# Kernel optimization log

Hardware: AMD Instinct MI355X
Metric: run time of the kernel (lower is better)

## Reference

```python
import jax, jax.numpy as jnp
import numpy as np
import itertools

F = 3          # num_sparse_features
C = 256        # num_categories
D = 64         # embedding_dim
H = 1024       # hidden_units
ND = 13        # num_dense_features
B = 16384      # batch
COMBOS = [c for r in range(2, F + 1) for c in itertools.combinations(range(F), r)]
WIDE_DIM = C * F + sum(C ** len(c) for c in COMBOS) + ND
DEEP_IN = F * D + ND


def setup_inputs() -> dict:
    key = jax.random.key(0)
    ks = jax.random.split(key, 12)
    sparse_inputs = jax.random.randint(ks[0], (B, F), 0, C, dtype=jnp.int32)
    dense_inputs = jax.random.normal(ks[1], (B, ND), dtype=jnp.float32)
    wide_w = jax.random.normal(ks[2], (WIDE_DIM,), dtype=jnp.float32) * 0.01
    wide_b = jax.random.normal(ks[3], (1,), dtype=jnp.float32) * 0.01
    emb = jax.random.normal(ks[4], (F, C, D), dtype=jnp.float32) * 0.05
    W1 = jax.random.normal(ks[5], (H, DEEP_IN), dtype=jnp.float32) / np.sqrt(DEEP_IN).astype(np.float32)
    b1 = jnp.zeros((H,), jnp.float32)
    W2 = jax.random.normal(ks[6], (H, H), dtype=jnp.float32) / np.sqrt(H).astype(np.float32)
    b2 = jnp.zeros((H,), jnp.float32)
    W3 = jax.random.normal(ks[7], (1, H), dtype=jnp.float32) / np.sqrt(H).astype(np.float32)
    b3 = jnp.zeros((1,), jnp.float32)
    return {"sparse_inputs": sparse_inputs, "dense_inputs": dense_inputs,
            "wide_w": wide_w, "wide_b": wide_b, "emb": emb,
            "W1": W1, "b1": b1, "W2": W2, "b2": b2, "W3": W3, "b3": b3}


def reference(sparse_inputs, dense_inputs, wide_w, wide_b, emb, W1, b1, W2, b2, W3, b3):
    # Wide path: one_hot(x) @ W.T  ==  gather of W columns at the hot indices.
    wide = wide_b[0]  # scalar, broadcasts to [B]
    for i in range(F):  # per-feature one-hot block, width C each
        wide = wide + wide_w[i * C + sparse_inputs[:, i]]
    off = F * C
    for combo in COMBOS:  # cross-feature one-hot blocks, width C**len(combo)
        cross = sparse_inputs[:, combo[0]]
        for j in combo[1:]:
            # faithful to source: multiplies by num_sparse_features (F), not C
            cross = cross * F + sparse_inputs[:, j]
        wide = wide + wide_w[off + cross]
        off += C ** len(combo)
    wide = wide + dense_inputs @ wide_w[off:off + ND]  # dense tail of wide linear
    wide = wide[:, None]  # [B, 1]

    # Deep path: per-feature embedding lookup -> concat -> 3-layer MLP
    embedded = jnp.concatenate([emb[i][sparse_inputs[:, i]] for i in range(F)], axis=1)  # [B, F*D]
    deep_x = jnp.concatenate([embedded, dense_inputs], axis=1)  # [B, DEEP_IN]
    h = jax.nn.relu(deep_x @ W1.T + b1)
    h = jax.nn.relu(h @ W2.T + b2)
    deep = h @ W3.T + b3  # [B, 1]

    return jax.nn.sigmoid(wide + deep)
```

## Files before the change

kernel.cpp:

```cpp
#include <hip/hip_runtime.h>
#include <stdint.h>


#define BATCH 16384
#define HDIM 1024
#define K1 256
#define DEEP_IN 205

typedef short bf16x8 __attribute__((ext_vector_type(8)));
typedef float f32x4 __attribute__((ext_vector_type(4)));
typedef uint16_t u16x8 __attribute__((ext_vector_type(8)));
typedef uint16_t u16x4 __attribute__((ext_vector_type(4)));

__device__ __forceinline__ uint16_t f2bf(float f) {
    uint32_t x;
    __builtin_memcpy(&x, &f, 4);
    uint32_t r = (x + 0x7fffu + ((x >> 16) & 1u)) >> 16;
    return (uint16_t)r;
}

__device__ __forceinline__ void async_ld16(const uint16_t* g, uint16_t* l) {
    __builtin_amdgcn_global_load_lds(
        (const __attribute__((address_space(1))) uint32_t*)g,
        (__attribute__((address_space(3))) uint32_t*)l, 16, 0, 0);
}

__global__ __launch_bounds__(256) void prep_kernel(
    const int* __restrict__ sp, const float* __restrict__ dense,
    const float* __restrict__ emb, const float* __restrict__ W1,
    const float* __restrict__ W2, const float* __restrict__ ww,
    const float* __restrict__ wb, const float* __restrict__ b3,
    uint16_t* __restrict__ embb, uint16_t* __restrict__ dtail,
    uint16_t* __restrict__ W1b, uint16_t* __restrict__ W2b,
    float* __restrict__ wide)
{
    const int bid = blockIdx.x;
    const int tid = threadIdx.x;
    if (bid < 24) {
        int k = bid * 256 + tid;
        const float* src = emb + (size_t)k * 8;
        float4 v0 = *(const float4*)src;
        float4 v1 = *(const float4*)(src + 4);
        u16x8 o;
        o[0] = f2bf(v0.x); o[1] = f2bf(v0.y); o[2] = f2bf(v0.z); o[3] = f2bf(v0.w);
        o[4] = f2bf(v1.x); o[5] = f2bf(v1.y); o[6] = f2bf(v1.z); o[7] = f2bf(v1.w);
        *(u16x8*)(embb + (size_t)k * 8) = o;
    } else if (bid < 536) {
        int idx = (bid - 24) * 256 + tid;
        int b = idx >> 3, c0 = (idx & 7) * 8;
        u16x8 o;
#pragma unroll
        for (int t = 0; t < 8; t++) {
            int c = c0 + t;
            o[t] = (c < 13) ? f2bf(dense[b * 13 + c]) : (uint16_t)0;
        }
        *(u16x8*)(dtail + (size_t)b * 64 + c0) = o;
    } else if (bid < 664) {
        int idx = (bid - 536) * 256 + tid;
        int n = idx >> 5, c0 = (idx & 31) * 8;
        u16x8 o;
#pragma unroll
        for (int t = 0; t < 8; t++) {
            int c = c0 + t;
            o[t] = (c < DEEP_IN) ? f2bf(W1[n * DEEP_IN + c]) : (uint16_t)0;
        }
        *(u16x8*)(W1b + (size_t)n * K1 + c0) = o;
    } else if (bid < 1176) {
        int k = (bid - 664) * 256 + tid;
        const float* src = W2 + (size_t)k * 8;
        float4 v0 = *(const float4*)src;
        float4 v1 = *(const float4*)(src + 4);
        u16x8 o;
        o[0] = f2bf(v0.x); o[1] = f2bf(v0.y); o[2] = f2bf(v0.z); o[3] = f2bf(v0.w);
        o[4] = f2bf(v1.x); o[5] = f2bf(v1.y); o[6] = f2bf(v1.z); o[7] = f2bf(v1.w);
        *(u16x8*)(W2b + (size_t)k * 8) = o;
    } else {
        int b = (bid - 1176) * 256 + tid;
        int s0 = sp[b * 3], s1 = sp[b * 3 + 1], s2 = sp[b * 3 + 2];
        float w = wb[0] + b3[0];
        w += ww[s0] + ww[256 + s1] + ww[512 + s2];
        w += ww[768    + s0 * 3 + s1];
        w += ww[66304  + s0 * 3 + s2];
        w += ww[131840 + s1 * 3 + s2];
        w += ww[197376 + (s0 * 3 + s1) * 3 + s2];
        const float* wd = ww + 16974592;
        float acc2 = 0.f;
#pragma unroll
        for (int j = 0; j < 13; j++) acc2 += dense[b * 13 + j] * wd[j];
        wide[b] = w + acc2;
    }
}

#define BAR8() do { asm volatile("" ::: "memory");                             \
    __builtin_amdgcn_s_barrier();                                              \
    asm volatile("" ::: "memory"); } while (0)
#define VM4() asm volatile("s_waitcnt vmcnt(4)" ::: "memory")
#define VM0() asm volatile("s_waitcnt vmcnt(0)" ::: "memory")

#define LDA8(base, msub) do {                                                  \
    _Pragma("unroll") for (int mt = 0; mt < 4; mt++) {                         \
        int ro_ = (base) + ((msub) * 64 + mt * 16) * 64;                       \
        af[mt][0] = *(const bf16x8*)&lds[ro_ + kc0];                           \
        af[mt][1] = *(const bf16x8*)&lds[ro_ + kc1];                           \
    } } while (0)

#define LDB8(dst, base, nsub) do {                                             \
    _Pragma("unroll") for (int nt = 0; nt < 2; nt++) {                         \
        int ro_ = (base) + ((nsub) * 32 + nt * 16) * 64;                       \
        dst[nt][0] = *(const bf16x8*)&lds[ro_ + kc0];                          \
        dst[nt][1] = *(const bf16x8*)&lds[ro_ + kc1];                          \
    } } while (0)

#define MM8(msub, nsub, BF) do {                                               \
    __builtin_amdgcn_s_setprio(1);                                             \
    _Pragma("unroll") for (int mt = 0; mt < 4; mt++)                           \
    _Pragma("unroll") for (int nt = 0; nt < 2; nt++) {                         \
        acc[(msub)*4+mt][(nsub)*2+nt] = __builtin_amdgcn_mfma_f32_16x16x32_bf16( \
            af[mt][0], BF[nt][0], acc[(msub)*4+mt][(nsub)*2+nt], 0, 0, 0);     \
        acc[(msub)*4+mt][(nsub)*2+nt] = __builtin_amdgcn_mfma_f32_16x16x32_bf16( \
            af[mt][1], BF[nt][1], acc[(msub)*4+mt][(nsub)*2+nt], 0, 0, 0);     \
    }                                                                          \
    __builtin_amdgcn_s_setprio(0); } while (0)

#define GEMM8_DECLS()                                                          \
    const int tid = threadIdx.x;                                               \
    const int lane = tid & 63, wave = tid >> 6;                                \
    const int wm = wave >> 2, wn = wave & 3;                                   \
    const int id = blockIdx.x;                                                 \
    const int wg = (id & 7) * 32 + (id >> 3);                                  \
    const int by = wg >> 2, bx = wg & 3;                                       \
    const int bm = by * 256, bn = bx * 256;                                    \
    const int lam = lane & 15, lad = lane >> 4;                                \
    const int sw = (lane & 7) << 4;                                            \
    const int kc0 = ((lad * 16) ^ sw) >> 1;                                    \
    const int kc1 = ((64 + lad * 16) ^ sw) >> 1;                               \
    const int aBE = wm * 8192 + lam * 64;                                      \
    const int aBO = aBE + 16384;                                               \
    const int bBE = 32768 + (wn >> 1) * 8192 + ((wn & 1) * 64 + lam) * 64;     \
    const int bBO = bBE + 16384;                                               \
    const int trow = tid >> 3;                                                 \
    const int csel = ((tid & 7) ^ (trow & 7)) << 3;

#define GEMM8_MAIN()                                                           \
    f32x4 acc[8][4];                                                           \
    _Pragma("unroll") for (int i = 0; i < 8; i++)                              \
        _Pragma("unroll") for (int j = 0; j < 4; j++) acc[i][j] = (f32x4)0.f;  \
    bf16x8 af[4][2], bf0[2][2], bf1[2][2];                                     \
    const int NT = K >> 6;                                                     \
    const int NI = K >> 7;                                                     \
    STG8A(0, 0, 0);     STG8A(0, 1, 0);                                        \
    STG8B(32768, 0, 0); STG8B(32768, 1, 0);                                    \
    STG8B(49152, 0, 64); STG8B(49152, 1, 64);                                  \
    VM4();                                                                     \
    BAR8();                                                                    \
    for (int it = 0; it < NI; ++it) {                                          \
        const int k1 = (2 * it + 1) * 64;                                      \
        const int t2 = 2 * it + 2, t3 = 2 * it + 3;                            \
        const int k2 = (t2 < NT ? t2 : 0) * 64;                                \
        const int k3 = (t3 < NT ? t3 : 0) * 64;                                \
        LDA8(aBE, 0); LDB8(bf0, bBE, 0); STG8A(16384, 0, k1);                  \
        BAR8(); MM8(0, 0, bf0); BAR8();                                        \
        LDB8(bf1, bBE, 1); STG8A(16384, 1, k1);                                \
        BAR8(); MM8(0, 1, bf1); BAR8();                                        \
        LDA8(aBE, 1); STG8B(32768, 0, k2);                                     \
        BAR8(); MM8(1, 1, bf1); BAR8();                                        \
        STG8B(32768, 1, k2);                                                   \
        BAR8(); MM8(1, 0, bf0); VM4(); BAR8();                                 \
        LDA8(aBO, 0); LDB8(bf0, bBO, 0); STG8A(0, 0, k2);                      \
        BAR8(); MM8(0, 0, bf0); BAR8();                                        \
        LDB8(bf1, bBO, 1); STG8A(0, 1, k2);                                    \
        BAR8(); MM8(0, 1, bf1); BAR8();                                        \
        LDA8(aBO, 1); STG8B(49152, 0, k3);                                     \
        BAR8(); MM8(1, 1, bf1); BAR8();                                        \
        STG8B(49152, 1, k3);                                                   \
        BAR8(); MM8(1, 0, bf0); VM4(); BAR8();                                 \
    }

#define ASRC1(pkv, h2, kt) ((kt) < 192                                         \
    ? (embb + (((kt) >> 6) << 14)                                              \
            + ((int)(((pkv) >> (((kt) >> 6) << 3)) & 255u) << 6) + csel)       \
    : (dtail + (size_t)(b0 + (h2) * 64) * 64 + csel))

#define STG8A(regoff, h, kt) do {                                              \
    async_ld16(ASRC1(PK##h##_0, 2*(h), kt),                                    \
               &lds[(regoff) + (h) * 8192 + wave * 512]);                      \
    async_ld16(ASRC1(PK##h##_1, 2*(h)+1, kt),                                  \
               &lds[(regoff) + (h) * 8192 + 4096 + wave * 512]);               \
} while (0)

#define STG8B(regoff, h, kt) do {                                              \
    const uint16_t* g_ = bRow + (size_t)((h) * 128) * (size_t)K + (kt);        \
    async_ld16(g_, &lds[(regoff) + (h) * 8192 + wave * 512]);                  \
    async_ld16(g_ + (size_t)64 * (size_t)K,                                    \
               &lds[(regoff) + (h) * 8192 + 4096 + wave * 512]);               \
} while (0)

__global__ __launch_bounds__(512, 2) void gemm1_8(
    const int* __restrict__ sp, const uint16_t* __restrict__ embb,
    const uint16_t* __restrict__ dtail, const uint16_t* __restrict__ Bw,
    const float* __restrict__ bias, uint16_t* __restrict__ C)
{
    __shared__ __align__(16) uint16_t lds[65536];
    GEMM8_DECLS()
    const int K = K1;
    const int b0 = bm + trow;
    const uint32_t PK0_0 = (uint32_t)sp[(b0      ) * 3] |
                           ((uint32_t)sp[(b0      ) * 3 + 1] << 8) |
                           ((uint32_t)sp[(b0      ) * 3 + 2] << 16);
    const uint32_t PK0_1 = (uint32_t)sp[(b0 +  64) * 3] |
                           ((uint32_t)sp[(b0 +  64) * 3 + 1] << 8) |
                           ((uint32_t)sp[(b0 +  64) * 3 + 2] << 16);
    const uint32_t PK1_0 = (uint32_t)sp[(b0 + 128) * 3] |
                           ((uint32_t)sp[(b0 + 128) * 3 + 1] << 8) |
                           ((uint32_t)sp[(b0 + 128) * 3 + 2] << 16);
    const uint32_t PK1_1 = (uint32_t)sp[(b0 + 192) * 3] |
                           ((uint32_t)sp[(b0 + 192) * 3 + 1] << 8) |
                           ((uint32_t)sp[(b0 + 192) * 3 + 2] << 16);
    const int prow = 4 * (trow & 15) + (trow >> 4);
    const uint16_t* bRow = Bw + (size_t)(bn + prow) * K + csel;
    VM0();
    GEMM8_MAIN()

    float bv[4];
#pragma unroll
    for (int jn = 0; jn < 4; jn++) bv[jn] = bias[bn + wn * 64 + 4 * lam + jn];
#pragma unroll
    for (int im = 0; im < 8; im++) {
#pragma unroll
        for (int r = 0; r < 4; r++) {
            int m = bm + wm * 128 + im * 16 + lad * 4 + r;
            u16x4 o;
#pragma unroll
            for (int jn = 0; jn < 4; jn++)
                o[jn] = f2bf(fmaxf(acc[im][jn][r] + bv[jn], 0.f));
            *(u16x4*)&C[(size_t)m * HDIM + bn + wn * 64 + 4 * lam] = o;
        }
    }
}

#undef STG8A
#undef STG8B

#define STG8A(regoff, h, kt) do {                                              \
    const uint16_t* g_ = aRow + (size_t)((h) * 128) * (size_t)K + (kt);        \
    async_ld16(g_, &lds[(regoff) + (h) * 8192 + wave * 512]);                  \
    async_ld16(g_ + (size_t)64 * (size_t)K,                                    \
               &lds[(regoff) + (h) * 8192 + 4096 + wave * 512]);               \
} while (0)

#define STG8B(regoff, h, kt) do {                                              \
    const uint16_t* g_ = bRow + (size_t)((h) * 128) * (size_t)K + (kt);        \
    async_ld16(g_, &lds[(regoff) + (h) * 8192 + wave * 512]);                  \
    async_ld16(g_ + (size_t)64 * (size_t)K,                                    \
               &lds[(regoff) + (h) * 8192 + 4096 + wave * 512]);               \
} while (0)

__global__ __launch_bounds__(512, 2) void gemm_fused8(
    const uint16_t* __restrict__ A, const uint16_t* __restrict__ Bw,
    const float* __restrict__ bias, const float* __restrict__ W3,
    float* __restrict__ outacc, int M, int N, int K)
{
    __shared__ __align__(16) uint16_t lds[65536];
    GEMM8_DECLS()
    const uint16_t* aRow = A + (size_t)(bm + trow) * K + csel;
    const uint16_t* bRow = Bw + (size_t)(bn + trow) * K + csel;
    GEMM8_MAIN()

    float bv[4], w3v[4];
#pragma unroll
    for (int jn = 0; jn < 4; jn++) {
        int n = bn + wn * 64 + jn * 16 + lam;
        bv[jn] = bias[n];
        w3v[jn] = W3[n];
    }
#pragma unroll
    for (int im = 0; im < 8; im++) {
#pragma unroll
        for (int r = 0; r < 4; r++) {
            float pt = 0.f;
#pragma unroll
            for (int jn = 0; jn < 4; jn++)
                pt += fmaxf(acc[im][jn][r] + bv[jn], 0.f) * w3v[jn];
            pt += __shfl_xor(pt, 1);
            pt += __shfl_xor(pt, 2);
            pt += __shfl_xor(pt, 4);
            pt += __shfl_xor(pt, 8);
            if (lam == 0) {
                int m = bm + wm * 128 + im * 16 + lad * 4 + r;
                atomicAdd(&outacc[m], pt);
            }
        }
    }
}

#undef STG8A
#undef STG8B

__global__ __launch_bounds__(256) void sigmoid_kernel(
    const float* __restrict__ outacc, float* __restrict__ out)
{
    int b = blockIdx.x * 256 + threadIdx.x;
    out[b] = 1.f / (1.f + __expf(-outacc[b]));
}

extern "C" void kernel_launch(void* const* d_in, const int* in_sizes, int n_in,
                              void* d_out, int out_size, void* d_ws, size_t ws_size,
                              hipStream_t stream) {
    const int*   sp    = (const int*)d_in[0];
    const float* dense = (const float*)d_in[1];
    const float* ww    = (const float*)d_in[2];
    const float* wb    = (const float*)d_in[3];
    const float* emb   = (const float*)d_in[4];
    const float* W1    = (const float*)d_in[5];
    const float* b1    = (const float*)d_in[6];
    const float* W2    = (const float*)d_in[7];
    const float* b2    = (const float*)d_in[8];
    const float* W3    = (const float*)d_in[9];
    const float* b3    = (const float*)d_in[10];
    float* out = (float*)d_out;

    char* ws = (char*)d_ws;
    float*    wide  = (float*)ws;
    uint16_t* embb  = (uint16_t*)(ws + 65536);
    uint16_t* dtail = (uint16_t*)(ws + 163840);
    uint16_t* W1b   = (uint16_t*)(ws + 2260992);
    uint16_t* W2b   = (uint16_t*)(ws + 2785280);
    uint16_t* h1    = (uint16_t*)(ws + 4882432);

    prep_kernel<<<1240, 256, 0, stream>>>(
        sp, dense, emb, W1, W2, ww, wb, b3, embb, dtail, W1b, W2b, wide);
    gemm1_8<<<256, 512, 0, stream>>>(
        sp, embb, dtail, W1b, b1, h1);
    gemm_fused8<<<256, 512, 0, stream>>>(
        h1, W2b, b2, W3, wide, BATCH, HDIM, HDIM);
    sigmoid_kernel<<<BATCH / 256, 256, 0, stream>>>(wide, out);
}
```

Measured before the change: 159.2 us.

## Fuse sigmoid into GEMM2 epilogue via last-block counter and LDS row reduction

Per-wave partial row sums are now reduced across the four column waves in LDS before a single atomicAdd per row, replacing many per-wave global atomics. A per-row-tile counter, zeroed in the prep kernel, identifies the last of the four column blocks, and that block applies the sigmoid and writes the output. This drops the separate sigmoid kernel launch. In exchange it adds two block barriers, a counter atomic, and an atomic read-back, and correctness depends on the memory ordering of the counter handshake.

Result: no change. 160.8 us (+1.0%).

```diff
diff --git a/kernel.cpp b/kernel.cpp
--- a/kernel.cpp
+++ b/kernel.cpp
@@ -32,7 +32,7 @@
     const float* __restrict__ wb, const float* __restrict__ b3,
     uint16_t* __restrict__ embb, uint16_t* __restrict__ dtail,
     uint16_t* __restrict__ W1b, uint16_t* __restrict__ W2b,
-    float* __restrict__ wide)
+    float* __restrict__ wide, int* __restrict__ cnt)
 {
     const int bid = blockIdx.x;
     const int tid = threadIdx.x;
@@ -74,7 +74,7 @@
         o[0] = f2bf(v0.x); o[1] = f2bf(v0.y); o[2] = f2bf(v0.z); o[3] = f2bf(v0.w);
         o[4] = f2bf(v1.x); o[5] = f2bf(v1.y); o[6] = f2bf(v1.z); o[7] = f2bf(v1.w);
         *(u16x8*)(W2b + (size_t)k * 8) = o;
-    } else {
+    } else if (bid < 1240) {
         int b = (bid - 1176) * 256 + tid;
         int s0 = sp[b * 3], s1 = sp[b * 3 + 1], s2 = sp[b * 3 + 2];
         float w = wb[0] + b3[0];
@@ -88,6 +88,8 @@
 #pragma unroll
         for (int j = 0; j < 13; j++) acc2 += dense[b * 13 + j] * wd[j];
         wide[b] = w + acc2;
+    } else {
+        if (tid < 64) cnt[tid] = 0;
     }
 }
 
@@ -258,9 +260,11 @@
 __global__ __launch_bounds__(512, 2) void gemm_fused8(
     const uint16_t* __restrict__ A, const uint16_t* __restrict__ Bw,
     const float* __restrict__ bias, const float* __restrict__ W3,
-    float* __restrict__ outacc, int M, int N, int K)
+    float* __restrict__ outacc, int* __restrict__ cnt,
+    float* __restrict__ out, int M, int N, int K)
 {
     __shared__ __align__(16) uint16_t lds[65536];
+    __shared__ int doneFlag;
     GEMM8_DECLS()
     const uint16_t* aRow = A + (size_t)(bm + trow) * K + csel;
     const uint16_t* bRow = Bw + (size_t)(bn + trow) * K + csel;
@@ -273,6 +277,8 @@
         bv[jn] = bias[n];
         w3v[jn] = W3[n];
     }
+    float* ldsF = (float*)lds;
+    __syncthreads();
 #pragma unroll
     for (int im = 0; im < 8; im++) {
 #pragma unroll
@@ -285,23 +291,28 @@
             pt += __shfl_xor(pt, 2);
             pt += __shfl_xor(pt, 4);
             pt += __shfl_xor(pt, 8);
-            if (lam == 0) {
-                int m = bm + wm * 128 + im * 16 + lad * 4 + r;
-                atomicAdd(&outacc[m], pt);
-            }
+            if (lam == 0)
+                ldsF[wn * 256 + wm * 128 + im * 16 + lad * 4 + r] = pt;
         }
+    }
+    __syncthreads();
+    if (tid < 256) {
+        float s = (ldsF[tid] + ldsF[256 + tid])
+                + (ldsF[512 + tid] + ldsF[768 + tid]);
+        atomicAdd(&outacc[bm + tid], s);
+    }
+    VM0();
+    __syncthreads();
+    if (tid == 0) doneFlag = atomicAdd(&cnt[by], 1);
+    __syncthreads();
+    if (doneFlag == 3 && tid < 256) {
+        float v = atomicAdd(&outacc[bm + tid], 0.f);
+        out[bm + tid] = 1.f / (1.f + __expf(-v));
     }
 }
 
 #undef STG8A
 #undef STG8B
-
-__global__ __launch_bounds__(256) void sigmoid_kernel(
-    const float* __restrict__ outacc, float* __restrict__ out)
-{
-    int b = blockIdx.x * 256 + threadIdx.x;
-    out[b] = 1.f / (1.f + __expf(-outacc[b]));
-}
 
 extern "C" void kernel_launch(void* const* d_in, const int* in_sizes, int n_in,
                               void* d_out, int out_size, void* d_ws, size_t ws_size,
@@ -326,12 +337,12 @@
     uint16_t* W1b   = (uint16_t*)(ws + 2260992);
     uint16_t* W2b   = (uint16_t*)(ws + 2785280);
     uint16_t* h1    = (uint16_t*)(ws + 4882432);
-
-    prep_kernel<<<1240, 256, 0, stream>>>(
-        sp, dense, emb, W1, W2, ww, wb, b3, embb, dtail, W1b, W2b, wide);
+    int*      cnt   = (int*)(ws + 38436864);
+
+    prep_kernel<<<1241, 256, 0, stream>>>(
+        sp, dense, emb, W1, W2, ww, wb, b3, embb, dtail, W1b, W2b, wide, cnt);
     gemm1_8<<<256, 512, 0, stream>>>(
         sp, embb, dtail, W1b, b1, h1);
     gemm_fused8<<<256, 512, 0, stream>>>(
-        h1, W2b, b2, W3, wide, BATCH, HDIM, HDIM);
-    sigmoid_kernel<<<BATCH / 256, 256, 0, stream>>>(wide, out);
-}
+        h1, W2b, b2, W3, wide, cnt, out, BATCH, HDIM, HDIM);
+}
```

## Restructure GEMM mainloop to 4-stage K=32 pipeline with new LDS swizzle

Applied to the files above, without the earlier changes.

Replaces the double-buffered K=64 tile mainloop with a 4-slot ring of K=32 tiles, prefetching three tiles ahead and waiting with vmcnt(8). The per-wave MFMA sub-block shape changes to 4x4 16x16 tiles per half, with a new XOR swizzle for LDS reads and global sources. The aim is deeper overlap of global-to-LDS async loads with MFMA work and fewer barriers per unit of K. In exchange, each iteration does half as much MFMA work per barrier pair, so synchronisation overhead per FLOP may rise.

After: 160.6 us. Within noise of the previous version (+0.8%).

```diff
diff --git a/kernel.cpp b/kernel.cpp
--- a/kernel.cpp
+++ b/kernel.cpp
@@ -94,35 +94,29 @@
 #define BAR8() do { asm volatile("" ::: "memory");                             \
     __builtin_amdgcn_s_barrier();                                              \
     asm volatile("" ::: "memory"); } while (0)
-#define VM4() asm volatile("s_waitcnt vmcnt(4)" ::: "memory")
+#define VM8() asm volatile("s_waitcnt vmcnt(8)" ::: "memory")
 #define VM0() asm volatile("s_waitcnt vmcnt(0)" ::: "memory")
 
-#define LDA8(base, msub) do {                                                  \
-    _Pragma("unroll") for (int mt = 0; mt < 4; mt++) {                         \
-        int ro_ = (base) + ((msub) * 64 + mt * 16) * 64;                       \
-        af[mt][0] = *(const bf16x8*)&lds[ro_ + kc0];                           \
-        af[mt][1] = *(const bf16x8*)&lds[ro_ + kc1];                           \
-    } } while (0)
-
-#define LDB8(dst, base, nsub) do {                                             \
-    _Pragma("unroll") for (int nt = 0; nt < 2; nt++) {                         \
-        int ro_ = (base) + ((nsub) * 32 + nt * 16) * 64;                       \
-        dst[nt][0] = *(const bf16x8*)&lds[ro_ + kc0];                          \
-        dst[nt][1] = *(const bf16x8*)&lds[ro_ + kc1];                          \
-    } } while (0)
-
-#define MM8(msub, nsub, BF) do {                                               \
+#define LDA4(sA, msub) do {                                                    \
+    _Pragma("unroll") for (int mt = 0; mt < 4; mt++)                           \
+        af[mt] = *(const bf16x8*)&lds[(sA) * 8192 + aOff                       \
+                                      + ((msub) * 64 + mt * 16) * 32];         \
+} while (0)
+
+#define LDB4(sB) do {                                                          \
+    _Pragma("unroll") for (int nt = 0; nt < 4; nt++)                           \
+        bf[nt] = *(const bf16x8*)&lds[32768 + (sB) * 8192 + bOff + nt * 512];  \
+} while (0)
+
+#define MM4(msub) do {                                                         \
     __builtin_amdgcn_s_setprio(1);                                             \
     _Pragma("unroll") for (int mt = 0; mt < 4; mt++)                           \
-    _Pragma("unroll") for (int nt = 0; nt < 2; nt++) {                         \
-        acc[(msub)*4+mt][(nsub)*2+nt] = __builtin_amdgcn_mfma_f32_16x16x32_bf16( \
-            af[mt][0], BF[nt][0], acc[(msub)*4+mt][(nsub)*2+nt], 0, 0, 0);     \
-        acc[(msub)*4+mt][(nsub)*2+nt] = __builtin_amdgcn_mfma_f32_16x16x32_bf16( \
-            af[mt][1], BF[nt][1], acc[(msub)*4+mt][(nsub)*2+nt], 0, 0, 0);     \
-    }                                                                          \
+    _Pragma("unroll") for (int nt = 0; nt < 4; nt++)                           \
+        acc[(msub) * 4 + mt][nt] = __builtin_amdgcn_mfma_f32_16x16x32_bf16(    \
+            af[mt], bf[nt], acc[(msub) * 4 + mt][nt], 0, 0, 0);                \
     __builtin_amdgcn_s_setprio(0); } while (0)
 
-#define GEMM8_DECLS()                                                          \
+#define GEMM4_DECLS()                                                          \
     const int tid = threadIdx.x;                                               \
     const int lane = tid & 63, wave = tid >> 6;                                \
     const int wm = wave >> 2, wn = wave & 3;                                   \
@@ -131,68 +125,46 @@
     const int by = wg >> 2, bx = wg & 3;                                       \
     const int bm = by * 256, bn = bx * 256;                                    \
     const int lam = lane & 15, lad = lane >> 4;                                \
-    const int sw = (lane & 7) << 4;                                            \
-    const int kc0 = ((lad * 16) ^ sw) >> 1;                                    \
-    const int kc1 = ((64 + lad * 16) ^ sw) >> 1;                               \
-    const int aBE = wm * 8192 + lam * 64;                                      \
-    const int aBO = aBE + 16384;                                               \
-    const int bBE = 32768 + (wn >> 1) * 8192 + ((wn & 1) * 64 + lam) * 64;     \
-    const int bBO = bBE + 16384;                                               \
-    const int trow = tid >> 3;                                                 \
-    const int csel = ((tid & 7) ^ (trow & 7)) << 3;
-
-#define GEMM8_MAIN()                                                           \
+    const int kce = (lad ^ ((lam >> 1) & 3)) * 8;    \
+    const int aOff = (wm * 128 + lam) * 32 + kce;                              \
+    const int bOff = (wn * 64 + lam) * 32 + kce;                               \
+    const int trow = tid >> 2;                                     \
+    const int gsrc = ((tid & 3) ^ ((tid >> 3) & 3)) * 8;
+
+#define GEMM4_MAIN(STA, STB)                                                   \
     f32x4 acc[8][4];                                                           \
     _Pragma("unroll") for (int i = 0; i < 8; i++)                              \
         _Pragma("unroll") for (int j = 0; j < 4; j++) acc[i][j] = (f32x4)0.f;  \
-    bf16x8 af[4][2], bf0[2][2], bf1[2][2];                                     \
-    const int NT = K >> 6;                                                     \
-    const int NI = K >> 7;                                                     \
-    STG8A(0, 0, 0);     STG8A(0, 1, 0);                                        \
-    STG8B(32768, 0, 0); STG8B(32768, 1, 0);                                    \
-    STG8B(49152, 0, 64); STG8B(49152, 1, 64);                                  \
-    VM4();                                                                     \
+    bf16x8 af[4], bf[4];                                                       \
+    const int NT = K >> 5;                                                     \
+    STA(0, 0);  STB(0, 0);                                                     \
+    STA(1, 32); STB(1, 32);                                                    \
+    STA(2, 64); STB(2, 64);                                                    \
+    VM8();                                                                     \
     BAR8();                                                                    \
-    for (int it = 0; it < NI; ++it) {                                          \
-        const int k1 = (2 * it + 1) * 64;                                      \
-        const int t2 = 2 * it + 2, t3 = 2 * it + 3;                            \
-        const int k2 = (t2 < NT ? t2 : 0) * 64;                                \
-        const int k3 = (t3 < NT ? t3 : 0) * 64;                                \
-        LDA8(aBE, 0); LDB8(bf0, bBE, 0); STG8A(16384, 0, k1);                  \
-        BAR8(); MM8(0, 0, bf0); BAR8();                                        \
-        LDB8(bf1, bBE, 1); STG8A(16384, 1, k1);                                \
-        BAR8(); MM8(0, 1, bf1); BAR8();                                        \
-        LDA8(aBE, 1); STG8B(32768, 0, k2);                                     \
-        BAR8(); MM8(1, 1, bf1); BAR8();                                        \
-        STG8B(32768, 1, k2);                                                   \
-        BAR8(); MM8(1, 0, bf0); VM4(); BAR8();                                 \
-        LDA8(aBO, 0); LDB8(bf0, bBO, 0); STG8A(0, 0, k2);                      \
-        BAR8(); MM8(0, 0, bf0); BAR8();                                        \
-        LDB8(bf1, bBO, 1); STG8A(0, 1, k2);                                    \
-        BAR8(); MM8(0, 1, bf1); BAR8();                                        \
-        LDA8(aBO, 1); STG8B(49152, 0, k3);                                     \
-        BAR8(); MM8(1, 1, bf1); BAR8();                                        \
-        STG8B(49152, 1, k3);                                                   \
-        BAR8(); MM8(1, 0, bf0); VM4(); BAR8();                                 \
-    }
-
-#define ASRC1(pkv, h2, kt) ((kt) < 192                                         \
+    for (int t = 0; t < NT; ++t) {                                             \
+        const int s = t & 3, s3 = (t + 3) & 3;                                 \
+        const int kt3 = (t + 3 < NT ? t + 3 : 0) << 5;                         \
+        LDA4(s, 0); LDB4(s); STA(s3, kt3);                                     \
+        BAR8(); MM4(0); BAR8();                                                \
+        LDA4(s, 1); STB(s3, kt3);                                              \
+        BAR8(); MM4(1); VM8(); BAR8();                                         \
+    }
+
+#define ASRC1(pk, b, kt) ((kt) < 192                                           \
     ? (embb + (((kt) >> 6) << 14)                                              \
-            + ((int)(((pkv) >> (((kt) >> 6) << 3)) & 255u) << 6) + csel)       \
-    : (dtail + (size_t)(b0 + (h2) * 64) * 64 + csel))
-
-#define STG8A(regoff, h, kt) do {                                              \
-    async_ld16(ASRC1(PK##h##_0, 2*(h), kt),                                    \
-               &lds[(regoff) + (h) * 8192 + wave * 512]);                      \
-    async_ld16(ASRC1(PK##h##_1, 2*(h)+1, kt),                                  \
-               &lds[(regoff) + (h) * 8192 + 4096 + wave * 512]);               \
-} while (0)
-
-#define STG8B(regoff, h, kt) do {                                              \
-    const uint16_t* g_ = bRow + (size_t)((h) * 128) * (size_t)K + (kt);        \
-    async_ld16(g_, &lds[(regoff) + (h) * 8192 + wave * 512]);                  \
-    async_ld16(g_ + (size_t)64 * (size_t)K,                                    \
-               &lds[(regoff) + (h) * 8192 + 4096 + wave * 512]);               \
+            + ((int)(((pk) >> (((kt) >> 6) << 3)) & 255u) << 6)                \
+            + ((kt) & 63) + gsrc)                                              \
+    : (dtail + (size_t)(b) * 64 + ((kt) - 192) + gsrc))
+
+#define STGA1(s, kt) do {                                                      \
+    async_ld16(ASRC1(PKa, b1, kt), &lds[(s) * 8192 + wave * 512]);             \
+    async_ld16(ASRC1(PKb, b2, kt), &lds[(s) * 8192 + 4096 + wave * 512]);      \
+} while (0)
+
+#define STGB1(s, kt) do {                                                      \
+    async_ld16(bR1 + (kt), &lds[32768 + (s) * 8192 + wave * 512]);             \
+    async_ld16(bR2 + (kt), &lds[32768 + (s) * 8192 + 4096 + wave * 512]);      \
 } while (0)
 
 __global__ __launch_bounds__(512, 2) void gemm1_8(
@@ -201,25 +173,22 @@
     const float* __restrict__ bias, uint16_t* __restrict__ C)
 {
     __shared__ __align__(16) uint16_t lds[65536];
-    GEMM8_DECLS()
+    GEMM4_DECLS()
     const int K = K1;
-    const int b0 = bm + trow;
-    const uint32_t PK0_0 = (uint32_t)sp[(b0      ) * 3] |
-                           ((uint32_t)sp[(b0      ) * 3 + 1] << 8) |
-                           ((uint32_t)sp[(b0      ) * 3 + 2] << 16);
-    const uint32_t PK0_1 = (uint32_t)sp[(b0 +  64) * 3] |
-                           ((uint32_t)sp[(b0 +  64) * 3 + 1] << 8) |
-                           ((uint32_t)sp[(b0 +  64) * 3 + 2] << 16);
-    const uint32_t PK1_0 = (uint32_t)sp[(b0 + 128) * 3] |
-                           ((uint32_t)sp[(b0 + 128) * 3 + 1] << 8) |
-                           ((uint32_t)sp[(b0 + 128) * 3 + 2] << 16);
-    const uint32_t PK1_1 = (uint32_t)sp[(b0 + 192) * 3] |
-                           ((uint32_t)sp[(b0 + 192) * 3 + 1] << 8) |
-                           ((uint32_t)sp[(b0 + 192) * 3 + 2] << 16);
-    const int prow = 4 * (trow & 15) + (trow >> 4);
-    const uint16_t* bRow = Bw + (size_t)(bn + prow) * K + csel;
+    const int b1 = bm + trow, b2 = bm + 128 + trow;
+    const uint32_t PKa = (uint32_t)sp[b1 * 3] |
+                         ((uint32_t)sp[b1 * 3 + 1] << 8) |
+                         ((uint32_t)sp[b1 * 3 + 2] << 16);
+    const uint32_t PKb = (uint32_t)sp[b2 * 3] |
+                         ((uint32_t)sp[b2 * 3 + 1] << 8) |
+                         ((uint32_t)sp[b2 * 3 + 2] << 16);
+    const int n1 = bn + (trow & 192) + 4 * (trow & 15) + ((trow >> 4) & 3);
+    const int r2v = 128 + trow;
+    const int n2 = bn + (r2v & 192) + 4 * (trow & 15) + ((trow >> 4) & 3);
+    const uint16_t* bR1 = Bw + (size_t)n1 * K + gsrc;
+    const uint16_t* bR2 = Bw + (size_t)n2 * K + gsrc;
     VM0();
-    GEMM8_MAIN()
+    GEMM4_MAIN(STGA1, STGB1)
 
     float bv[4];
 #pragma unroll
@@ -238,21 +207,17 @@
     }
 }
 
-#undef STG8A
-#undef STG8B
-
-#define STG8A(regoff, h, kt) do {                                              \
-    const uint16_t* g_ = aRow + (size_t)((h) * 128) * (size_t)K + (kt);        \
-    async_ld16(g_, &lds[(regoff) + (h) * 8192 + wave * 512]);                  \
-    async_ld16(g_ + (size_t)64 * (size_t)K,                                    \
-               &lds[(regoff) + (h) * 8192 + 4096 + wave * 512]);               \
-} while (0)
-
-#define STG8B(regoff, h, kt) do {                                              \
-    const uint16_t* g_ = bRow + (size_t)((h) * 128) * (size_t)K + (kt);        \
-    async_ld16(g_, &lds[(regoff) + (h) * 8192 + wave * 512]);                  \
-    async_ld16(g_ + (size_t)64 * (size_t)K,                                    \
-               &lds[(regoff) + (h) * 8192 + 4096 + wave * 512]);               \
+#undef STGA1
+#undef STGB1
+
+#define STGA2(s, kt) do {                                                      \
+    async_ld16(aR1 + (kt), &lds[(s) * 8192 + wave * 512]);                     \
+    async_ld16(aR2 + (kt), &lds[(s) * 8192 + 4096 + wave * 512]);              \
+} while (0)
+
+#define STGB2(s, kt) do {                                                      \
+    async_ld16(bR1 + (kt), &lds[32768 + (s) * 8192 + wave * 512]);             \
+    async_ld16(bR2 + (kt), &lds[32768 + (s) * 8192 + 4096 + wave * 512]);      \
 } while (0)
 
 __global__ __launch_bounds__(512, 2) void gemm_fused8(
@@ -261,10 +226,12 @@
     float* __restrict__ outacc, int M, int N, int K)
 {
     __shared__ __align__(16) uint16_t lds[65536];
-    GEMM8_DECLS()
-    const uint16_t* aRow = A + (size_t)(bm + trow) * K + csel;
-    const uint16_t* bRow = Bw + (size_t)(bn + trow) * K + csel;
-    GEMM8_MAIN()
+    GEMM4_DECLS()
+    const uint16_t* aR1 = A + (size_t)(bm + trow) * K + gsrc;
+    const uint16_t* aR2 = A + (size_t)(bm + 128 + trow) * K + gsrc;
+    const uint16_t* bR1 = Bw + (size_t)(bn + trow) * K + gsrc;
+    const uint16_t* bR2 = Bw + (size_t)(bn + 128 + trow) * K + gsrc;
+    GEMM4_MAIN(STGA2, STGB2)
 
     float bv[4], w3v[4];
 #pragma unroll
@@ -293,8 +260,8 @@
     }
 }
 
-#undef STG8A
-#undef STG8B
+#undef STGA2
+#undef STGB2
 
 __global__ __launch_bounds__(256) void sigmoid_kernel(
     const float* __restrict__ outacc, float* __restrict__ out)
```

## Load W2 B-fragments directly from global to registers in fused GEMM2

Applied to the files above, without the earlier changes.

In the second GEMM kernel, the B operand (W2) is no longer staged through LDS. Each wave now loads its own B fragments straight from global memory into registers, and LDS holds only the double-buffered A tiles, which halves its allocation. This removes LDS traffic and async copies for B and frees LDS space. The cost is uncoalesced global loads of W2, which now sit on the critical path before the MFMAs. It also relies on the L2 cache, because four waves along M read the same rows.

Result: slower. 186.2 us (+17.0%).

```diff
diff --git a/kernel.cpp b/kernel.cpp
--- a/kernel.cpp
+++ b/kernel.cpp
@@ -122,11 +122,11 @@
     }                                                                          \
     __builtin_amdgcn_s_setprio(0); } while (0)
 
-#define GEMM8_DECLS()                                                          \
+#define GEMM8_DECLS(BID)                                                       \
     const int tid = threadIdx.x;                                               \
     const int lane = tid & 63, wave = tid >> 6;                                \
     const int wm = wave >> 2, wn = wave & 3;                                   \
-    const int id = blockIdx.x;                                                 \
+    const int id = (BID);                                                      \
     const int wg = (id & 7) * 32 + (id >> 3);                                  \
     const int by = wg >> 2, bx = wg & 3;                                       \
     const int bm = by * 256, bn = bx * 256;                                    \
@@ -201,7 +201,7 @@
     const float* __restrict__ bias, uint16_t* __restrict__ C)
 {
     __shared__ __align__(16) uint16_t lds[65536];
-    GEMM8_DECLS()
+    GEMM8_DECLS(blockIdx.x)
     const int K = K1;
     const int b0 = bm + trow;
     const uint32_t PK0_0 = (uint32_t)sp[(b0      ) * 3] |
@@ -241,18 +241,25 @@
 #undef STG8A
 #undef STG8B
 
-#define STG8A(regoff, h, kt) do {                                              \
+#define STA2(regoff, h, kt) do {                                               \
     const uint16_t* g_ = aRow + (size_t)((h) * 128) * (size_t)K + (kt);        \
     async_ld16(g_, &lds[(regoff) + (h) * 8192 + wave * 512]);                  \
     async_ld16(g_ + (size_t)64 * (size_t)K,                                    \
                &lds[(regoff) + (h) * 8192 + 4096 + wave * 512]);               \
 } while (0)
 
-#define STG8B(regoff, h, kt) do {                                              \
-    const uint16_t* g_ = bRow + (size_t)((h) * 128) * (size_t)K + (kt);        \
-    async_ld16(g_, &lds[(regoff) + (h) * 8192 + wave * 512]);                  \
-    async_ld16(g_ + (size_t)64 * (size_t)K,                                    \
-               &lds[(regoff) + (h) * 8192 + 4096 + wave * 512]);               \
+#define LDBG0(d, kt) do {                                                      \
+    d[0][0] = *(const bf16x8*)(bN0 + (kt));                                    \
+    d[0][1] = *(const bf16x8*)(bN0 + (kt) + 32);                               \
+    d[1][0] = *(const bf16x8*)(bN1 + (kt));                                    \
+    d[1][1] = *(const bf16x8*)(bN1 + (kt) + 32);                               \
+} while (0)
+
+#define LDBG1(d, kt) do {                                                      \
+    d[0][0] = *(const bf16x8*)(bN2 + (kt));                                    \
+    d[0][1] = *(const bf16x8*)(bN2 + (kt) + 32);                               \
+    d[1][0] = *(const bf16x8*)(bN3 + (kt));                                    \
+    d[1][1] = *(const bf16x8*)(bN3 + (kt) + 32);                               \
 } while (0)
 
 __global__ __launch_bounds__(512, 2) void gemm_fused8(
@@ -260,11 +267,47 @@
     const float* __restrict__ bias, const float* __restrict__ W3,
     float* __restrict__ outacc, int M, int N, int K)
 {
-    __shared__ __align__(16) uint16_t lds[65536];
-    GEMM8_DECLS()
+    __shared__ __align__(16) uint16_t lds[32768];
+    GEMM8_DECLS(blockIdx.x)
+    (void)bBE; (void)bBO;
     const uint16_t* aRow = A + (size_t)(bm + trow) * K + csel;
-    const uint16_t* bRow = Bw + (size_t)(bn + trow) * K + csel;
-    GEMM8_MAIN()
+    const uint16_t* bN0 = Bw + (size_t)(bn + wn * 64 + lam) * K + lad * 8;
+    const uint16_t* bN1 = bN0 + (size_t)16 * K;
+    const uint16_t* bN2 = bN0 + (size_t)32 * K;
+    const uint16_t* bN3 = bN0 + (size_t)48 * K;
+
+    f32x4 acc[8][4];
+#pragma unroll
+    for (int i = 0; i < 8; i++)
+#pragma unroll
+        for (int j = 0; j < 4; j++) acc[i][j] = (f32x4)0.f;
+    bf16x8 af[4][2], bf0[2][2], bf1[2][2];
+    const int NI = K >> 7;
+
+    STA2(0, 0, 0); STA2(0, 1, 0);
+    VM0();
+    BAR8();
+
+    for (int it = 0; it < NI; ++it) {
+        const int ktE = it << 7, ktO = ktE + 64;
+        const int ktN = (it + 1 < NI) ? (ktE + 128) : 0;
+        LDBG0(bf0, ktE); LDBG1(bf1, ktE);
+        STA2(16384, 0, ktO); STA2(16384, 1, ktO);
+        LDA8(aBE, 0);
+        BAR8(); MM8(0, 0, bf0); BAR8();
+        BAR8(); MM8(0, 1, bf1); BAR8();
+        LDA8(aBE, 1);
+        BAR8(); MM8(1, 1, bf1); BAR8();
+        BAR8(); MM8(1, 0, bf0); VM0(); BAR8();
+        LDBG0(bf0, ktO); LDBG1(bf1, ktO);
+        STA2(0, 0, ktN); STA2(0, 1, ktN);
+        LDA8(aBO, 0);
+        BAR8(); MM8(0, 0, bf0); BAR8();
+        BAR8(); MM8(0, 1, bf1); BAR8();
+        LDA8(aBO, 1);
+        BAR8(); MM8(1, 1, bf1); BAR8();
+        BAR8(); MM8(1, 0, bf0); VM0(); BAR8();
+    }
 
     float bv[4], w3v[4];
 #pragma unroll
@@ -293,8 +336,9 @@
     }
 }
 
-#undef STG8A
-#undef STG8B
+#undef STA2
+#undef LDBG0
+#undef LDBG1
 
 __global__ __launch_bounds__(256) void sigmoid_kernel(
     const float* __restrict__ outacc, float* __restrict__ out)
```
